# Kernel tuning notes

Hardware: AMD Instinct MI355X
Metric: run time of the kernel (lower is better)

The kernel has to match this reference:

```python
import jax, jax.numpy as jnp
import numpy as np

N = 50000   # nodes
E = 800000  # edges
B = 512     # graphs
EPS = 1e-5  # BatchNorm eps


def _p(k, shape, scale=0.05):
    return jax.random.normal(k, shape, dtype=jnp.float32) * scale


def setup_inputs() -> dict:
    key = jax.random.key(0)
    ks = jax.random.split(key, 24)
    inp = {
        "x": jax.random.normal(ks[0], (N, 4), dtype=jnp.float32),
        "edge_index": jax.random.randint(ks[1], (2, E), 0, N, dtype=jnp.int64),
        "edge_weight": jax.random.uniform(ks[2], (E,), dtype=jnp.float32),
        "batch": jnp.sort(jax.random.randint(ks[3], (N,), 0, B, dtype=jnp.int64)),
        # block1: GCNConv(4,64) + BN + shortcut Linear(4,64)
        "W1": _p(ks[4], (4, 64)), "b1": jnp.zeros((64,), jnp.float32),
        "g1": jnp.ones((64,), jnp.float32), "be1": jnp.zeros((64,), jnp.float32),
        "sW1": _p(ks[5], (4, 64)), "sb1": jnp.zeros((64,), jnp.float32),
        # block2: GCNConv(64,64) + BN, identity shortcut
        "W2": _p(ks[6], (64, 64)), "b2": jnp.zeros((64,), jnp.float32),
        "g2": jnp.ones((64,), jnp.float32), "be2": jnp.zeros((64,), jnp.float32),
        # block3: GCNConv(64,128) + BN + shortcut Linear(64,128)
        "W3": _p(ks[7], (64, 128)), "b3": jnp.zeros((128,), jnp.float32),
        "g3": jnp.ones((128,), jnp.float32), "be3": jnp.zeros((128,), jnp.float32),
        "sW3": _p(ks[8], (64, 128)), "sb3": jnp.zeros((128,), jnp.float32),
        # head: Linear(256,128) + BN + ReLU + Linear(128,1)
        "fW1": _p(ks[9], (256, 128)), "fb1": jnp.zeros((128,), jnp.float32),
        "fg": jnp.ones((128,), jnp.float32), "fbe": jnp.zeros((128,), jnp.float32),
        "fW2": _p(ks[10], (128, 1)), "fb2": jnp.zeros((1,), jnp.float32),
    }
    return inp


def _bn(x, g, b):
    # training-mode BatchNorm1d over node dim (biased variance)
    m = x.mean(0)
    v = x.var(0)
    return (x - m) * jax.lax.rsqrt(v + EPS) * g + b


def _gcn(x, W, b, src, dst, w, n):
    # PyG GCNConv: add self-loops (weight 1), symmetric normalization
    h = x @ W  # [n, out]
    loop = jnp.arange(n)
    s = jnp.concatenate([src, loop])
    d = jnp.concatenate([dst, loop])
    ww = jnp.concatenate([w, jnp.ones((n,), x.dtype)])
    deg = jax.ops.segment_sum(ww, d, num_segments=n)
    dis = jnp.where(deg > 0, jax.lax.rsqrt(jnp.maximum(deg, EPS)), 0.0)
    norm = dis[s] * ww * dis[d]  # [E+n]
    return jax.ops.segment_sum(h[s] * norm[:, None], d, num_segments=n) + b


def _block(x, W, b, g, be, sW, sb, src, dst, w, n):
    out = jax.nn.relu(_bn(_gcn(x, W, b, src, dst, w, n), g, be))
    sc = x if sW is None else x @ sW + sb
    return out + sc


def reference(x, edge_index, edge_weight, batch,
              W1, b1, g1, be1, sW1, sb1,
              W2, b2, g2, be2,
              W3, b3, g3, be3, sW3, sb3,
              fW1, fb1, fg, fbe, fW2, fb2):
    n = x.shape[0]
    src, dst = edge_index[0], edge_index[1]
    h = _block(x, W1, b1, g1, be1, sW1, sb1, src, dst, edge_weight, n)
    h = _block(h, W2, b2, g2, be2, None, None, src, dst, edge_weight, n)
    h = _block(h, W3, b3, g3, be3, sW3, sb3, src, dst, edge_weight, n)
    # global mean / max pooling per graph
    cnt = jax.ops.segment_sum(jnp.ones((n,), h.dtype), batch, num_segments=B)
    p1 = jax.ops.segment_sum(h, batch, num_segments=B) / jnp.maximum(cnt, 1.0)[:, None]
    p2 = jax.ops.segment_max(h, batch, num_segments=B)
    z = jnp.concatenate([p1, p2], axis=1)  # [B, 256]
    z = jax.nn.relu(_bn(z @ fW1 + fb1, fg, fbe))  # Dropout eval = identity
    return z @ fW2 + fb2  # [B, 1]
```

## Files before the change

kernel.cpp:

```cpp
#include <hip/hip_runtime.h>

#define BNEPS 1e-5f


__global__ void k_fill(float* p, int n, float v){
  int i = blockIdx.x*blockDim.x + threadIdx.x;
  if(i < n) p[i] = v;
}


__global__ void k_count(int* cnt, float* deg, const int* __restrict__ dst,
                        const float* __restrict__ w, int E){
  int e = blockIdx.x*blockDim.x + threadIdx.x;
  if(e < E){
    int d = dst[e];
    atomicAdd(&cnt[d], 1);
    atomicAdd(&deg[d], w[e]);
  }
}

__global__ void k_scan1(int* cnt, float* dis, int* rowptr, int* bsum, int n){
  __shared__ int sh[256];
  int tid = threadIdx.x;
  int i = blockIdx.x*256 + tid;
  int v = (i < n) ? cnt[i] : 0;
  sh[tid] = v;
  __syncthreads();
  for(int o = 1; o < 256; o <<= 1){
    int t = (tid >= o) ? sh[tid-o] : 0;
    __syncthreads();
    sh[tid] += t;
    __syncthreads();
  }
  if(i < n){
    rowptr[i] = sh[tid] - v;
    cnt[i] = 0;
    dis[i] = rsqrtf(1.f + dis[i]);
  }
  if(tid == 255) bsum[blockIdx.x] = sh[255];
}

__global__ void k_scan2(int* bsum, int m){
  __shared__ int sh[256];
  int tid = threadIdx.x;
  int v = (tid < m) ? bsum[tid] : 0;
  sh[tid] = v;
  __syncthreads();
  for(int o = 1; o < 256; o <<= 1){
    int t = (tid >= o) ? sh[tid-o] : 0;
    __syncthreads();
    sh[tid] += t;
    __syncthreads();
  }
  if(tid < m) bsum[tid] = sh[tid] - v;
}

__global__ void k_scan3(int* rowptr, const int* bsum, int n, int E){
  int i = blockIdx.x*blockDim.x + threadIdx.x;
  if(i < n) rowptr[i] += bsum[i >> 8];
  if(i == 0) rowptr[n] = E;
}

__global__ void k_scatter2(const int* __restrict__ src, const int* __restrict__ dst,
                           const float* __restrict__ w, const int* __restrict__ rowptr,
                           int* cur, const float* __restrict__ dis,
                           int2* __restrict__ erec, int E){
  int e = blockIdx.x*blockDim.x + threadIdx.x;
  if(e >= E) return;
  int d = dst[e];
  int s = src[e];
  int idx = rowptr[d] + atomicAdd(&cur[d], 1);
  float nm = dis[s] * w[e] * dis[d];
  erec[idx] = make_int2(s, __float_as_int(nm));
}


__global__ __launch_bounds__(256)
void k_gcn1_fused(const float* __restrict__ X, const float* __restrict__ dis,
                  const int* __restrict__ rowptr, const int2* __restrict__ erec,
                  const float* __restrict__ W, const float* __restrict__ bias,
                  float* __restrict__ H, float* __restrict__ stats, int n){
  const int tid = threadIdx.x;
  const int lane = tid & 63;
  const int wid = tid >> 6;
  const int eg = lane >> 2;
  const int ch = lane & 3;
  const float w0 = W[lane], w1 = W[64+lane], w2 = W[128+lane], w3 = W[192+lane];
  const float bc = bias[lane];
  float s = 0.f, s2 = 0.f;
  for(int i = blockIdx.x*4 + wid; i < n; i += gridDim.x*4){
    int e0 = rowptr[i], e1 = rowptr[i+1];
    float acc = 0.f;
    for(int j = e0 + eg; j < e1; j += 16){
      int2 r = erec[j];
      acc += X[(size_t)r.x*4 + ch] * __int_as_float(r.y);
    }
    if(eg == 0){
      float d = dis[i];
      acc += X[(size_t)i*4 + ch] * d * d;
    }
    acc += __shfl_xor(acc, 4);
    acc += __shfl_xor(acc, 8);
    acc += __shfl_xor(acc, 16);
    acc += __shfl_xor(acc, 32);
    float p0 = __shfl(acc, 0), p1 = __shfl(acc, 1);
    float p2 = __shfl(acc, 2), p3 = __shfl(acc, 3);
    float h = bc + p0*w0 + p1*w1 + p2*w2 + p3*w3;
    H[(size_t)i*64 + lane] = h;
    s += h; s2 += h*h;
  }
  __shared__ float rs[256], rs2[256];
  rs[tid] = s; rs2[tid] = s2;
  __syncthreads();
  if(tid < 64){
    atomicAdd(&stats[tid],    rs[tid]+rs[tid+64]+rs[tid+128]+rs[tid+192]);
    atomicAdd(&stats[64+tid], rs2[tid]+rs2[tid+64]+rs2[tid+128]+rs2[tid+192]);
  }
}


template<int C>
__global__ void k_gather(const float* __restrict__ H, const float* __restrict__ dis,
                         const int* __restrict__ rowptr, const int2* __restrict__ erec,
                         float* __restrict__ P, int n){
  const int NPB = 256 / C;
  int i = blockIdx.x*NPB + threadIdx.x / C;
  int c = threadIdx.x % C;
  if(i >= n) return;
  float di = dis[i];
  float acc = H[(size_t)i*C + c]*di*di;
  int e0 = rowptr[i], e1 = rowptr[i+1];
  int j = e0;
  for(; j + 8 <= e1; j += 8){
    int2 r0 = erec[j],   r1 = erec[j+1], r2 = erec[j+2], r3 = erec[j+3];
    int2 r4 = erec[j+4], r5 = erec[j+5], r6 = erec[j+6], r7 = erec[j+7];
    float h0 = H[(size_t)r0.x*C + c];
    float h1 = H[(size_t)r1.x*C + c];
    float h2 = H[(size_t)r2.x*C + c];
    float h3 = H[(size_t)r3.x*C + c];
    float h4 = H[(size_t)r4.x*C + c];
    float h5 = H[(size_t)r5.x*C + c];
    float h6 = H[(size_t)r6.x*C + c];
    float h7 = H[(size_t)r7.x*C + c];
    acc += h0*__int_as_float(r0.y) + h1*__int_as_float(r1.y)
         + h2*__int_as_float(r2.y) + h3*__int_as_float(r3.y)
         + h4*__int_as_float(r4.y) + h5*__int_as_float(r5.y)
         + h6*__int_as_float(r6.y) + h7*__int_as_float(r7.y);
  }
  for(; j < e1; j++){
    int2 r = erec[j];
    acc += H[(size_t)r.x*C + c] * __int_as_float(r.y);
  }
  P[(size_t)i*C + c] = acc;
}


template<int C>
__global__ __launch_bounds__(256)
void k_gemm_tile(const float* __restrict__ X, const float* __restrict__ W,
                 const float* __restrict__ bias, float* __restrict__ H,
                 float* __restrict__ stats, int n, int ntiles){
  const int RR = C/16;
  const int CG = C/4;
  __shared__ float Xs[64*65];
  __shared__ float Ws[64*C];
  __shared__ float sst[2*C];
  const int tid = threadIdx.x;
  const int cg = tid % CG, rg = tid / CG;
  const int c0 = cg*4;
  for(int t = tid; t < 16*C; t += 256)
    reinterpret_cast<float4*>(Ws)[t] = reinterpret_cast<const float4*>(W)[t];
  const float4 bc = *reinterpret_cast<const float4*>(bias + c0);
  float sacc[4] = {0,0,0,0}, qacc[4] = {0,0,0,0};
  const float4* X4 = reinterpret_cast<const float4*>(X);
  for(int tile = blockIdx.x; tile < ntiles; tile += gridDim.x){
    const int r0 = tile*64;
    __syncthreads();
    #pragma unroll
    for(int q = 0; q < 4; q++){
      int idx = tid + q*256;
      int row = idx >> 4, k4 = idx & 15;
      float4 v = (r0+row < n) ? X4[(size_t)(r0+row)*16 + k4] : make_float4(0.f,0.f,0.f,0.f);
      Xs[(4*k4+0)*65 + row] = v.x;
      Xs[(4*k4+1)*65 + row] = v.y;
      Xs[(4*k4+2)*65 + row] = v.z;
      Xs[(4*k4+3)*65 + row] = v.w;
    }
    __syncthreads();
    float acc[RR][4];
    #pragma unroll
    for(int r = 0; r < RR; r++){ acc[r][0]=bc.x; acc[r][1]=bc.y; acc[r][2]=bc.z; acc[r][3]=bc.w; }
    #pragma unroll 8
    for(int k = 0; k < 64; k++){
      float4 wv = reinterpret_cast<const float4*>(Ws)[k*CG + cg];
      #pragma unroll
      for(int r = 0; r < RR; r++){
        float xv = Xs[k*65 + rg*RR + r];
        acc[r][0] = fmaf(xv, wv.x, acc[r][0]);
        acc[r][1] = fmaf(xv, wv.y, acc[r][1]);
        acc[r][2] = fmaf(xv, wv.z, acc[r][2]);
        acc[r][3] = fmaf(xv, wv.w, acc[r][3]);
      }
    }
    #pragma unroll
    for(int r = 0; r < RR; r++){
      int row = r0 + rg*RR + r;
      if(row < n){
        *reinterpret_cast<float4*>(H + (size_t)row*C + c0) =
            make_float4(acc[r][0], acc[r][1], acc[r][2], acc[r][3]);
        #pragma unroll
        for(int j = 0; j < 4; j++){ sacc[j] += acc[r][j]; qacc[j] += acc[r][j]*acc[r][j]; }
      }
    }
  }
  for(int t = tid; t < 2*C; t += 256) sst[t] = 0.f;
  __syncthreads();
  #pragma unroll
  for(int j = 0; j < 4; j++){
    atomicAdd(&sst[c0+j], sacc[j]);
    atomicAdd(&sst[C+c0+j], qacc[j]);
  }
  __syncthreads();
  for(int t = tid; t < 2*C; t += 256) atomicAdd(&stats[t], sst[t]);
}

template<int C>
__global__ __launch_bounds__(256)
void k_gemm_bnsc_tile(const float* __restrict__ X, const float* __restrict__ sW,
                      const float* __restrict__ sb,
                      const float* __restrict__ agg, const float* __restrict__ stats,
                      const float* __restrict__ g, const float* __restrict__ be,
                      float* __restrict__ out, int n, int ntiles){
  const int RR = C/16;
  const int CG = C/4;
  __shared__ float Xs[64*65];
  __shared__ float Ws[64*C];
  const int tid = threadIdx.x;
  const int cg = tid % CG, rg = tid / CG;
  const int c0 = cg*4;
  for(int t = tid; t < 16*C; t += 256)
    reinterpret_cast<float4*>(Ws)[t] = reinterpret_cast<const float4*>(sW)[t];
  const float4 bc = *reinterpret_cast<const float4*>(sb + c0);
  float scal[4], shft[4];
  {
    float invn = 1.0f / n;
    #pragma unroll
    for(int j = 0; j < 4; j++){
      float m = stats[c0+j]*invn;
      float v = stats[C+c0+j]*invn - m*m;
      float rs = rsqrtf(v + BNEPS) * g[c0+j];
      scal[j] = rs;
      shft[j] = be[c0+j] - m*rs;
    }
  }
  const float4* X4 = reinterpret_cast<const float4*>(X);
  for(int tile = blockIdx.x; tile < ntiles; tile += gridDim.x){
    const int r0 = tile*64;
    __syncthreads();
    #pragma unroll
    for(int q = 0; q < 4; q++){
      int idx = tid + q*256;
      int row = idx >> 4, k4 = idx & 15;
      float4 v = (r0+row < n) ? X4[(size_t)(r0+row)*16 + k4] : make_float4(0.f,0.f,0.f,0.f);
      Xs[(4*k4+0)*65 + row] = v.x;
      Xs[(4*k4+1)*65 + row] = v.y;
      Xs[(4*k4+2)*65 + row] = v.z;
      Xs[(4*k4+3)*65 + row] = v.w;
    }
    __syncthreads();
    float acc[RR][4];
    #pragma unroll
    for(int r = 0; r < RR; r++){ acc[r][0]=bc.x; acc[r][1]=bc.y; acc[r][2]=bc.z; acc[r][3]=bc.w; }
    #pragma unroll 8
    for(int k = 0; k < 64; k++){
      float4 wv = reinterpret_cast<const float4*>(Ws)[k*CG + cg];
      #pragma unroll
      for(int r = 0; r < RR; r++){
        float xv = Xs[k*65 + rg*RR + r];
        acc[r][0] = fmaf(xv, wv.x, acc[r][0]);
        acc[r][1] = fmaf(xv, wv.y, acc[r][1]);
        acc[r][2] = fmaf(xv, wv.z, acc[r][2]);
        acc[r][3] = fmaf(xv, wv.w, acc[r][3]);
      }
    }
    #pragma unroll
    for(int r = 0; r < RR; r++){
      int row = r0 + rg*RR + r;
      if(row < n){
        float4 a = *reinterpret_cast<const float4*>(agg + (size_t)row*C + c0);
        float4 o;
        o.x = fmaxf(a.x*scal[0] + shft[0], 0.f) + acc[r][0];
        o.y = fmaxf(a.y*scal[1] + shft[1], 0.f) + acc[r][1];
        o.z = fmaxf(a.z*scal[2] + shft[2], 0.f) + acc[r][2];
        o.w = fmaxf(a.w*scal[3] + shft[3], 0.f) + acc[r][3];
        *reinterpret_cast<float4*>(out + (size_t)row*C + c0) = o;
      }
    }
  }
}


template<int C>
__global__ void k_bn_add4(const float* __restrict__ agg, const float* __restrict__ stats,
                          const float* __restrict__ g, const float* __restrict__ be,
                          const float* __restrict__ add, float* __restrict__ out, int n){
  int idx = blockIdx.x*blockDim.x + threadIdx.x;
  if(idx >= n*(C/4)) return;
  int c = (idx % (C/4))*4;
  float invn = 1.0f / n;
  float4 sm = *reinterpret_cast<const float4*>(stats + c);
  float4 sq = *reinterpret_cast<const float4*>(stats + C + c);
  float4 g4 = *reinterpret_cast<const float4*>(g + c);
  float4 b4 = *reinterpret_cast<const float4*>(be + c);
  float4 a  = reinterpret_cast<const float4*>(agg)[idx];
  float4 ad = reinterpret_cast<const float4*>(add)[idx];
  float4 o;
  #define BN1(X) { float m = sm.X*invn; float v = sq.X*invn - m*m; \
    o.X = fmaxf((a.X-m)*rsqrtf(v+BNEPS)*g4.X + b4.X, 0.f) + ad.X; }
  BN1(x) BN1(y) BN1(z) BN1(w)
  #undef BN1
  reinterpret_cast<float4*>(out)[idx] = o;
}

__global__ void k_bn_sc4_v4(const float* __restrict__ agg, const float* __restrict__ stats,
                            const float* __restrict__ g, const float* __restrict__ be,
                            const float* __restrict__ X, const float* __restrict__ sW,
                            const float* __restrict__ sb, float* __restrict__ out, int n){
  int idx = blockIdx.x*blockDim.x + threadIdx.x;
  if(idx >= n*16) return;
  int i = idx >> 4;
  int c = (idx & 15)*4;
  float invn = 1.0f / n;
  float4 xr = *reinterpret_cast<const float4*>(X + (size_t)i*4);
  float4 s0 = *reinterpret_cast<const float4*>(sW + c);
  float4 s1 = *reinterpret_cast<const float4*>(sW + 64 + c);
  float4 s2 = *reinterpret_cast<const float4*>(sW + 128 + c);
  float4 s3 = *reinterpret_cast<const float4*>(sW + 192 + c);
  float4 sb4 = *reinterpret_cast<const float4*>(sb + c);
  float4 sm = *reinterpret_cast<const float4*>(stats + c);
  float4 sq = *reinterpret_cast<const float4*>(stats + 64 + c);
  float4 g4 = *reinterpret_cast<const float4*>(g + c);
  float4 b4 = *reinterpret_cast<const float4*>(be + c);
  float4 a  = reinterpret_cast<const float4*>(agg)[idx];
  float4 o;
  #define BN1(X) { float sc = xr.x*s0.X + xr.y*s1.X + xr.z*s2.X + xr.w*s3.X + sb4.X; \
    float m = sm.X*invn; float v = sq.X*invn - m*m; \
    o.X = fmaxf((a.X-m)*rsqrtf(v+BNEPS)*g4.X + b4.X, 0.f) + sc; }
  BN1(x) BN1(y) BN1(z) BN1(w)
  #undef BN1
  reinterpret_cast<float4*>(out)[idx] = o;
}


__global__ void k_pool(const float* __restrict__ H, const int* __restrict__ batch,
                       float* __restrict__ z, int n){
  int b = blockIdx.x, c = threadIdx.x;
  int lo = 0, hi = n;
  while(lo < hi){ int mid = (lo+hi)>>1; if(batch[mid] <  b) lo = mid+1; else hi = mid; }
  int start = lo;
  hi = n;
  while(lo < hi){ int mid = (lo+hi)>>1; if(batch[mid] <  b+1) lo = mid+1; else hi = mid; }
  int end = lo;
  float s = 0.f, mx = -INFINITY;
  for(int i = start; i < end; i++){
    float v = H[(size_t)i*128 + c];
    s += v; mx = fmaxf(mx, v);
  }
  int cnt = end - start;
  z[b*256 + c]       = s / fmaxf((float)cnt, 1.f);
  z[b*256 + 128 + c] = mx;
}

__global__ void k_head1(const float* __restrict__ z, const float* __restrict__ fW1,
                        const float* __restrict__ fb1, float* __restrict__ zr,
                        float* __restrict__ stats, int B){
  int idx = blockIdx.x*blockDim.x + threadIdx.x;
  int tid = threadIdx.x;
  float acc = 0.f;
  if(idx < B*128){
    int b = idx >> 7, c = idx & 127;
    acc = fb1[c];
    #pragma unroll 4
    for(int k = 0; k < 256; k++) acc = fmaf(z[b*256+k], fW1[k*128+c], acc);
    zr[idx] = acc;
  }
  __shared__ float rs[256], rs2[256];
  rs[tid] = acc; rs2[tid] = acc*acc;
  __syncthreads();
  if(tid < 128){
    atomicAdd(&stats[tid],     rs[tid]+rs[tid+128]);
    atomicAdd(&stats[128+tid], rs2[tid]+rs2[tid+128]);
  }
}

__global__ void k_final(const float* __restrict__ zr, const float* __restrict__ stats,
                        const float* __restrict__ fg, const float* __restrict__ fbe,
                        const float* __restrict__ fW2, const float* __restrict__ fb2,
                        float* __restrict__ out, int B){
  __shared__ float red[128];
  int b = blockIdx.x, c = threadIdx.x;
  float invn = 1.0f / B;
  float m  = stats[c]*invn;
  float v  = stats[128+c]*invn - m*m;
  float rs = rsqrtf(v + BNEPS);
  float val = fmaxf((zr[b*128+c]-m)*rs*fg[c] + fbe[c], 0.f) * fW2[c];
  red[c] = val;
  __syncthreads();
  for(int s = 64; s > 0; s >>= 1){
    if(c < s) red[c] += red[c+s];
    __syncthreads();
  }
  if(c == 0) out[b] = red[0] + fb2[0];
}


extern "C" void kernel_launch(void* const* d_in, const int* in_sizes, int n_in,
                              void* d_out, int out_size, void* d_ws, size_t ws_size,
                              hipStream_t stream){
  const float* x   = (const float*)d_in[0];
  const int*   ei  = (const int*)  d_in[1];
  const float* ew  = (const float*)d_in[2];
  const int*   bat = (const int*)  d_in[3];
  const float* W1  = (const float*)d_in[4];  const float* b1  = (const float*)d_in[5];
  const float* g1  = (const float*)d_in[6];  const float* be1 = (const float*)d_in[7];
  const float* sW1 = (const float*)d_in[8];  const float* sb1 = (const float*)d_in[9];
  const float* W2  = (const float*)d_in[10]; const float* b2  = (const float*)d_in[11];
  const float* g2  = (const float*)d_in[12]; const float* be2 = (const float*)d_in[13];
  const float* W3  = (const float*)d_in[14]; const float* b3  = (const float*)d_in[15];
  const float* g3  = (const float*)d_in[16]; const float* be3 = (const float*)d_in[17];
  const float* sW3 = (const float*)d_in[18]; const float* sb3 = (const float*)d_in[19];
  const float* fW1 = (const float*)d_in[20]; const float* fb1 = (const float*)d_in[21];
  const float* fg  = (const float*)d_in[22]; const float* fbe = (const float*)d_in[23];
  const float* fW2 = (const float*)d_in[24]; const float* fb2 = (const float*)d_in[25];
  float* out = (float*)d_out;

  const int n = in_sizes[0] / 4;
  const int E = in_sizes[2];
  const int B = out_size;
  const int* src = ei;
  const int* dst = ei + E;

  auto GB = [](long long t){ return (int)((t + 255) / 256); };
  const int nscanb = (n + 255) / 256;
  const int ntiles = (n + 63) / 64;

  float* ws = (float*)d_ws;
  size_t off = 0;
  auto alloc = [&](size_t cnt)->float*{ float* p = ws + off; off += (cnt + 63) & ~size_t(63); return p; };

  const size_t npad = ((size_t)n + 63) & ~size_t(63);
  float* bufA  = alloc((size_t)n * 64);
  float* hbuf  = alloc((size_t)n * 128);
  float* agg   = alloc((size_t)n * 128);
  float* z     = alloc((size_t)B * 256);
  float* zr    = alloc((size_t)B * 128);
  float* zreg  = alloc(2*npad + 1024);
  int*   cnt   = (int*)zreg;
  float* dis   = zreg + npad;
  float* st1 = zreg + 2*npad; float* st2 = st1 + 256;
  float* st3 = st2 + 256;     float* stH = st3 + 256;
  int*   rowptr = (int*)alloc(n + 1);
  int*   bsum   = (int*)alloc(256);
  int2*  erec   = (int2*)alloc((size_t)E * 2);

  k_fill<<<GB(2*npad + 1024),256,0,stream>>>(zreg, (int)(2*npad + 1024), 0.f);
  k_count<<<GB(E),256,0,stream>>>(cnt, dis, dst, ew, E);
  k_scan1<<<nscanb,256,0,stream>>>(cnt, dis, rowptr, bsum, n);
  k_scan2<<<1,256,0,stream>>>(bsum, nscanb);
  k_scan3<<<GB(n),256,0,stream>>>(rowptr, bsum, n, E);
  k_scatter2<<<GB(E),256,0,stream>>>(src, dst, ew, rowptr, cnt, dis, erec, E);

  float* P = hbuf;
  k_gcn1_fused<<<512,256,0,stream>>>(x, dis, rowptr, erec, W1, b1, agg, st1, n);
  k_bn_sc4_v4<<<GB((long long)n*16),256,0,stream>>>(agg, st1, g1, be1, x, sW1, sb1, bufA, n);

  k_gather<64><<<(n+3)/4,256,0,stream>>>(bufA, dis, rowptr, erec, P, n);
  k_gemm_tile<64><<<512,256,0,stream>>>(P, W2, b2, agg, st2, n, ntiles);
  k_bn_add4<64><<<GB((long long)n*16),256,0,stream>>>(agg, st2, g2, be2, bufA, bufA, n);

  k_gather<64><<<(n+3)/4,256,0,stream>>>(bufA, dis, rowptr, erec, P, n);
  k_gemm_tile<128><<<512,256,0,stream>>>(P, W3, b3, agg, st3, n, ntiles);
  k_gemm_bnsc_tile<128><<<512,256,0,stream>>>(bufA, sW3, sb3, agg, st3, g3, be3, hbuf, n, ntiles);

  k_pool<<<B,128,0,stream>>>(hbuf, bat, z, n);
  k_head1<<<GB((long long)B*128),256,0,stream>>>(z, fW1, fb1, zr, stH, B);
  k_final<<<B,128,0,stream>>>(zr, stH, fg, fbe, fW2, fb2, out, B);
}
```

Before: 506.9 us.

## Compute degrees from CSR segments instead of float atomics

Removes the float atomicAdd for weighted degree from the edge-count pass. The scatter now stores raw edge weights, and two new per-node kernels follow it: one sums each CSR row to get deg^-1/2, the other rewrites the stored weights into normalized coefficients. This trades one float atomic per edge for two extra launches and thread-per-row loops that make non-coalesced reads and write-back over the edge records, with imbalance from varying row lengths. Summing each row in a fixed order also makes the degree deterministic.

After: 487.5 us. 1.04x faster.

```diff
diff --git a/kernel.cpp b/kernel.cpp
--- a/kernel.cpp
+++ b/kernel.cpp
@@ -9,17 +9,12 @@
 }
 
 
-__global__ void k_count(int* cnt, float* deg, const int* __restrict__ dst,
-                        const float* __restrict__ w, int E){
+__global__ void k_count(int* cnt, const int* __restrict__ dst, int E){
   int e = blockIdx.x*blockDim.x + threadIdx.x;
-  if(e < E){
-    int d = dst[e];
-    atomicAdd(&cnt[d], 1);
-    atomicAdd(&deg[d], w[e]);
-  }
-}
-
-__global__ void k_scan1(int* cnt, float* dis, int* rowptr, int* bsum, int n){
+  if(e < E) atomicAdd(&cnt[dst[e]], 1);
+}
+
+__global__ void k_scan1(int* cnt, int* rowptr, int* bsum, int n){
   __shared__ int sh[256];
   int tid = threadIdx.x;
   int i = blockIdx.x*256 + tid;
@@ -32,11 +27,7 @@
     sh[tid] += t;
     __syncthreads();
   }
-  if(i < n){
-    rowptr[i] = sh[tid] - v;
-    cnt[i] = 0;
-    dis[i] = rsqrtf(1.f + dis[i]);
-  }
+  if(i < n){ rowptr[i] = sh[tid] - v; cnt[i] = 0; }
   if(tid == 255) bsum[blockIdx.x] = sh[255];
 }
 
@@ -63,15 +54,34 @@
 
 __global__ void k_scatter2(const int* __restrict__ src, const int* __restrict__ dst,
                            const float* __restrict__ w, const int* __restrict__ rowptr,
-                           int* cur, const float* __restrict__ dis,
-                           int2* __restrict__ erec, int E){
+                           int* cur, int2* __restrict__ erec, int E){
   int e = blockIdx.x*blockDim.x + threadIdx.x;
   if(e >= E) return;
   int d = dst[e];
-  int s = src[e];
   int idx = rowptr[d] + atomicAdd(&cur[d], 1);
-  float nm = dis[s] * w[e] * dis[d];
-  erec[idx] = make_int2(s, __float_as_int(nm));
+  erec[idx] = make_int2(src[e], __float_as_int(w[e]));
+}
+
+__global__ void k_degdis(const int2* __restrict__ erec, const int* __restrict__ rowptr,
+                         float* __restrict__ dis, int n){
+  int i = blockIdx.x*blockDim.x + threadIdx.x;
+  if(i >= n) return;
+  float s = 1.0f;
+  int e0 = rowptr[i], e1 = rowptr[i+1];
+  for(int j = e0; j < e1; j++) s += __int_as_float(erec[j].y);
+  dis[i] = rsqrtf(s);
+}
+
+__global__ void k_mknorm(int2* __restrict__ erec, const int* __restrict__ rowptr,
+                         const float* __restrict__ dis, int n){
+  int i = blockIdx.x*blockDim.x + threadIdx.x;
+  if(i >= n) return;
+  float di = dis[i];
+  int e0 = rowptr[i], e1 = rowptr[i+1];
+  for(int j = e0; j < e1; j++){
+    int2 r = erec[j];
+    erec[j].y = __float_as_int(dis[r.x] * __int_as_float(r.y) * di);
+  }
 }
 
 
@@ -454,21 +464,23 @@
   float* agg   = alloc((size_t)n * 128);
   float* z     = alloc((size_t)B * 256);
   float* zr    = alloc((size_t)B * 128);
-  float* zreg  = alloc(2*npad + 1024);
+  float* zreg  = alloc(npad + 1024);
   int*   cnt   = (int*)zreg;
-  float* dis   = zreg + npad;
-  float* st1 = zreg + 2*npad; float* st2 = st1 + 256;
-  float* st3 = st2 + 256;     float* stH = st3 + 256;
+  float* st1 = zreg + npad; float* st2 = st1 + 256;
+  float* st3 = st2 + 256;   float* stH = st3 + 256;
+  float* dis    = alloc(n);
   int*   rowptr = (int*)alloc(n + 1);
   int*   bsum   = (int*)alloc(256);
   int2*  erec   = (int2*)alloc((size_t)E * 2);
 
-  k_fill<<<GB(2*npad + 1024),256,0,stream>>>(zreg, (int)(2*npad + 1024), 0.f);
-  k_count<<<GB(E),256,0,stream>>>(cnt, dis, dst, ew, E);
-  k_scan1<<<nscanb,256,0,stream>>>(cnt, dis, rowptr, bsum, n);
+  k_fill<<<GB(npad + 1024),256,0,stream>>>(zreg, (int)(npad + 1024), 0.f);
+  k_count<<<GB(E),256,0,stream>>>(cnt, dst, E);
+  k_scan1<<<nscanb,256,0,stream>>>(cnt, rowptr, bsum, n);
   k_scan2<<<1,256,0,stream>>>(bsum, nscanb);
   k_scan3<<<GB(n),256,0,stream>>>(rowptr, bsum, n, E);
-  k_scatter2<<<GB(E),256,0,stream>>>(src, dst, ew, rowptr, cnt, dis, erec, E);
+  k_scatter2<<<GB(E),256,0,stream>>>(src, dst, ew, rowptr, cnt, erec, E);
+  k_degdis<<<GB(n),256,0,stream>>>(erec, rowptr, dis, n);
+  k_mknorm<<<GB(n),256,0,stream>>>(erec, rowptr, dis, n);
 
   float* P = hbuf;
   k_gcn1_fused<<<512,256,0,stream>>>(x, dis, rowptr, erec, W1, b1, agg, st1, n);
```
